# Optimization experiments

Measured on AMD Instinct MI355X. Metric: run time of the kernel, lower is better.

The kernel has to match this reference:

```python
import jax, jax.numpy as jnp
import numpy as np

N_LHB = 2097152
N_MHB = 1048576
T = 20
# Izhikevich 'RS' parameters (standard regular-spiking cell)
A, B, C, D = 0.02, 0.2, -65.0, 8.0
V_PEAK = 30.0
I_TONIC = -1.0          # set via .fill_(-1.0) in __init__
RATE_DECAY = 0.9        # EMA decay assumed for IzhikevichLayer.rate buffer
THRESH, DECAY, GAIN = 0.4, 0.998, 0.05


def setup_inputs() -> dict:
    key = jax.random.key(0)
    k1, k2 = jax.random.split(key)
    return {
        "reward": jnp.float32(0.1),
        "expected_reward": jnp.float32(0.5),
        "aversion": jnp.float32(0.3),
        "DA": jnp.float32(0.5),
        "current_goal": 1,
        "frustration": jnp.full((4,), 0.2, jnp.float32),
        "v_lhb": jnp.full((N_LHB,), C, jnp.float32),
        "u_lhb": jnp.full((N_LHB,), B * C, jnp.float32),
        "rate_lhb": jnp.zeros((N_LHB,), jnp.float32),
        "v_mhb": jnp.full((N_MHB,), C, jnp.float32),
        "u_mhb": jnp.full((N_MHB,), B * C, jnp.float32),
        "rate_mhb": jnp.zeros((N_MHB,), jnp.float32),
        "noise_lhb": jax.random.normal(k1, (T, N_LHB), jnp.float32),
        "noise_mhb": jax.random.normal(k2, (T, N_MHB), jnp.float32),
    }


def _izhikevich_run(v, u, rate, noise, i_drive):
    """Run T Izhikevich steps with per-step noise. noise: [T, n]."""
    def step(carry, n_t):
        v, u, rate = carry
        I = i_drive + I_TONIC + n_t * 0.5
        v1 = v + (0.04 * v * v + 5.0 * v + 140.0 - u + I)
        u1 = u + A * (B * v - u)
        spike = (v1 >= V_PEAK).astype(jnp.float32)
        v2 = jnp.where(spike > 0.0, C, v1)
        u2 = jnp.where(spike > 0.0, u1 + D, u1)
        rate2 = rate * RATE_DECAY + spike * (1.0 - RATE_DECAY)
        return (v2, u2, rate2), None
    (v, u, rate), _ = jax.lax.scan(step, (v, u, rate), noise)
    return rate


def reference(reward, expected_reward, aversion, DA, current_goal, frustration,
              v_lhb, u_lhb, rate_lhb, v_mhb, u_mhb, rate_mhb,
              noise_lhb, noise_mhb):
    rpe = reward - expected_reward
    disappoint = jnp.maximum(0.0, -rpe)

    rate_l = _izhikevich_run(v_lhb, u_lhb, rate_lhb, noise_lhb, disappoint * 20.0)
    rate_m = _izhikevich_run(v_mhb, u_mhb, rate_mhb, noise_mhb, aversion * 15.0)

    lhb_mean = rate_l.mean()
    mhb_mean = rate_m.mean()
    da_supp = jnp.minimum(0.5, lhb_mean * 5.0)
    ht5_supp = jnp.minimum(0.3, lhb_mean * 3.0)

    # frustration / helplessness bookkeeping (cooldown assumed 0)
    f = frustration * DECAY
    f = f.at[current_goal].add(jnp.where(rpe < -0.05, GAIN * jnp.abs(rpe), 0.0))
    f = f.at[current_goal].multiply(jnp.where(rpe > 0.1, 0.8, 1.0))
    f = jnp.clip(f, 0.0, 1.0)
    helplessness = f.max()
    switch = (f[current_goal] > THRESH).astype(jnp.float32)
    f = f.at[current_goal].multiply(jnp.where(switch > 0.0, 0.3, 1.0))

    dopa_mod = jnp.maximum(0.5, 2.0 * (1.0 - DA))
    goal_bias = f * 0.5 * dopa_mod
    explore = jnp.minimum(1.0, disappoint * 2.0 + lhb_mean * 3.0)

    scalars = jnp.stack([disappoint, da_supp, ht5_supp, lhb_mean, mhb_mean,
                         explore, helplessness, switch])
    return jnp.concatenate([scalars, goal_bias, f])  # [16]
```

## Files before the change

### kernel.cpp

```cpp
#include <hip/hip_runtime.h>

constexpr int   T       = 20;
constexpr int   N_LHB   = 2097152;
constexpr int   N_MHB   = 1048576;
constexpr float PA      = 0.02f;
constexpr float PB      = 0.2f;
constexpr float PC      = -65.0f;
constexpr float PD      = 8.0f;
constexpr float V_PEAK  = 30.0f;
constexpr float I_TONIC = -1.0f;
constexpr float RDECAY  = 0.9f;
constexpr float THRESH  = 0.4f;
constexpr float DECAY   = 0.998f;
constexpr float GAIN    = 0.05f;

constexpr int BLK   = 256;
constexpr int NB_L  = N_LHB / 4 / BLK;
constexpr int NB_M  = N_MHB / 4 / BLK;

__device__ __forceinline__ void izh_step(float& v, float& u, float& rate, float I) {
    float v1 = v + (0.04f * v * v + 5.0f * v + 140.0f - u + I);
    float u1 = u + PA * (PB * v - u);
    bool spike = (v1 >= V_PEAK);
    v = spike ? PC : v1;
    u = spike ? (u1 + PD) : u1;
    rate = rate * RDECAY + (spike ? (1.0f - RDECAY) : 0.0f);
}

__global__ __launch_bounds__(BLK) void izh_fused(
    const float* __restrict__ reward, const float* __restrict__ expected,
    const float* __restrict__ aversion,
    const float* __restrict__ v_l, const float* __restrict__ u_l, const float* __restrict__ r_l,
    const float* __restrict__ v_m, const float* __restrict__ u_m, const float* __restrict__ r_m,
    const float* __restrict__ noise_l, const float* __restrict__ noise_m,
    float* __restrict__ partial)
{
    const int bid = blockIdx.x;
    const int tid = threadIdx.x;

    const float* vv; const float* uu; const float* rr; const float* nz;
    int n4, i;
    float drive;
    if (bid < NB_L) {
        n4 = N_LHB / 4;
        i  = bid * BLK + tid;
        vv = v_l; uu = u_l; rr = r_l; nz = noise_l;
        drive = fmaxf(0.0f, expected[0] - reward[0]) * 20.0f;
    } else {
        n4 = N_MHB / 4;
        i  = (bid - NB_L) * BLK + tid;
        vv = v_m; uu = u_m; rr = r_m; nz = noise_m;
        drive = aversion[0] * 15.0f;
    }
    drive += I_TONIC;

    float4 v = ((const float4*)vv)[i];
    float4 u = ((const float4*)uu)[i];
    float4 r = ((const float4*)rr)[i];

    #pragma unroll
    for (int t = 0; t < T; ++t) {
        float4 n = ((const float4*)nz)[(size_t)t * n4 + i];
        izh_step(v.x, u.x, r.x, drive + n.x * 0.5f);
        izh_step(v.y, u.y, r.y, drive + n.y * 0.5f);
        izh_step(v.z, u.z, r.z, drive + n.z * 0.5f);
        izh_step(v.w, u.w, r.w, drive + n.w * 0.5f);
    }

    float s = (r.x + r.y) + (r.z + r.w);
    #pragma unroll
    for (int o = 32; o > 0; o >>= 1) s += __shfl_down(s, o, 64);

    __shared__ float sh[4];
    if ((tid & 63) == 0) sh[tid >> 6] = s;
    __syncthreads();
    if (tid == 0) partial[bid] = (sh[0] + sh[1]) + (sh[2] + sh[3]);
}

__global__ __launch_bounds__(BLK) void finalize(
    const float* __restrict__ partial,
    const float* __restrict__ reward, const float* __restrict__ expected,
    const float* __restrict__ aversion, const float* __restrict__ da,
    const int* __restrict__ goal, const float* __restrict__ frustration,
    float* __restrict__ out)
{
    const int tid = threadIdx.x;
    float sl = 0.0f, sm = 0.0f;
    for (int i = tid; i < NB_L; i += BLK) sl += partial[i];
    for (int i = tid; i < NB_M; i += BLK) sm += partial[NB_L + i];
    #pragma unroll
    for (int o = 32; o > 0; o >>= 1) {
        sl += __shfl_down(sl, o, 64);
        sm += __shfl_down(sm, o, 64);
    }
    __shared__ float sh[8];
    if ((tid & 63) == 0) { sh[tid >> 6] = sl; sh[4 + (tid >> 6)] = sm; }
    __syncthreads();

    if (tid == 0) {
        float lhb_sum = (sh[0] + sh[1]) + (sh[2] + sh[3]);
        float mhb_sum = (sh[4] + sh[5]) + (sh[6] + sh[7]);
        float lhb_mean = lhb_sum / (float)N_LHB;
        float mhb_mean = mhb_sum / (float)N_MHB;

        float rpe = reward[0] - expected[0];
        float disappoint = fmaxf(0.0f, -rpe);
        float da_supp = fminf(0.5f, lhb_mean * 5.0f);
        float ht5_supp = fminf(0.3f, lhb_mean * 3.0f);

        int g = goal[0];
        float f[4];
        #pragma unroll
        for (int k = 0; k < 4; ++k) f[k] = frustration[k] * DECAY;
        f[g] += (rpe < -0.05f) ? GAIN * fabsf(rpe) : 0.0f;
        f[g] *= (rpe > 0.1f) ? 0.8f : 1.0f;
        #pragma unroll
        for (int k = 0; k < 4; ++k) f[k] = fminf(1.0f, fmaxf(0.0f, f[k]));
        float helplessness = fmaxf(fmaxf(f[0], f[1]), fmaxf(f[2], f[3]));
        float sw = (f[g] > THRESH) ? 1.0f : 0.0f;
        f[g] *= (sw > 0.0f) ? 0.3f : 1.0f;

        float dopa_mod = fmaxf(0.5f, 2.0f * (1.0f - da[0]));
        float explore = fminf(1.0f, disappoint * 2.0f + lhb_mean * 3.0f);

        out[0] = disappoint;
        out[1] = da_supp;
        out[2] = ht5_supp;
        out[3] = lhb_mean;
        out[4] = mhb_mean;
        out[5] = explore;
        out[6] = helplessness;
        out[7] = sw;
        #pragma unroll
        for (int k = 0; k < 4; ++k) out[8 + k] = f[k] * 0.5f * dopa_mod;
        #pragma unroll
        for (int k = 0; k < 4; ++k) out[12 + k] = f[k];
    }
}

extern "C" void kernel_launch(void* const* d_in, const int* in_sizes, int n_in,
                              void* d_out, int out_size, void* d_ws, size_t ws_size,
                              hipStream_t stream) {
    const float* reward      = (const float*)d_in[0];
    const float* expected    = (const float*)d_in[1];
    const float* aversion    = (const float*)d_in[2];
    const float* da          = (const float*)d_in[3];
    const int*   goal        = (const int*)d_in[4];
    const float* frustration = (const float*)d_in[5];
    const float* v_l         = (const float*)d_in[6];
    const float* u_l         = (const float*)d_in[7];
    const float* r_l         = (const float*)d_in[8];
    const float* v_m         = (const float*)d_in[9];
    const float* u_m         = (const float*)d_in[10];
    const float* r_m         = (const float*)d_in[11];
    const float* noise_l     = (const float*)d_in[12];
    const float* noise_m     = (const float*)d_in[13];

    float* out     = (float*)d_out;
    float* partial = (float*)d_ws;

    izh_fused<<<NB_L + NB_M, BLK, 0, stream>>>(
        reward, expected, aversion,
        v_l, u_l, r_l, v_m, u_m, r_m,
        noise_l, noise_m, partial);

    finalize<<<1, BLK, 0, stream>>>(
        partial, reward, expected, aversion, da, goal, frustration, out);
}
```

Before: 58.46 us.

## Process eight neurons per thread, prefetch noise, and aggregate rate sums algebraically

Each thread now handles two float4 groups, which halves the block count. Noise loads are software-prefetched three timesteps ahead in registers to overlap memory latency with compute. The per-neuron rate EMA is replaced by a single per-thread EMA over the spike count, which is valid because the EMA is linear. The Izhikevich update is refactored into FMAs with folded constants. These changes cut ALU work and lengthen the memory pipeline, but they raise register pressure and may change floating-point rounding slightly.

```diff
diff --git a/kernel.cpp b/kernel.cpp
--- a/kernel.cpp
+++ b/kernel.cpp
@@ -3,28 +3,27 @@
 constexpr int   T       = 20;
 constexpr int   N_LHB   = 2097152;
 constexpr int   N_MHB   = 1048576;
-constexpr float PA      = 0.02f;
-constexpr float PB      = 0.2f;
-constexpr float PC      = -65.0f;
-constexpr float PD      = 8.0f;
 constexpr float V_PEAK  = 30.0f;
 constexpr float I_TONIC = -1.0f;
-constexpr float RDECAY  = 0.9f;
 constexpr float THRESH  = 0.4f;
 constexpr float DECAY   = 0.998f;
 constexpr float GAIN    = 0.05f;
 
-constexpr int BLK   = 256;
-constexpr int NB_L  = N_LHB / 4 / BLK;
-constexpr int NB_M  = N_MHB / 4 / BLK;
+constexpr int BLK  = 256;
+constexpr int VEC  = 8;
+constexpr int NB_L = N_LHB / (VEC * BLK);
+constexpr int NB_M = N_MHB / (VEC * BLK);
+constexpr int PF   = 3;
 
-__device__ __forceinline__ void izh_step(float& v, float& u, float& rate, float I) {
-    float v1 = v + (0.04f * v * v + 5.0f * v + 140.0f - u + I);
-    float u1 = u + PA * (PB * v - u);
-    bool spike = (v1 >= V_PEAK);
-    v = spike ? PC : v1;
-    u = spike ? (u1 + PD) : u1;
-    rate = rate * RDECAY + (spike ? (1.0f - RDECAY) : 0.0f);
+__device__ __forceinline__ float istep(float& v, float& u, float n, float c) {
+    float q  = fmaf(0.5f, n, c) - u;
+    float p  = fmaf(0.04f, v, 6.0f);
+    float v1 = fmaf(v, p, q);
+    float u1 = fmaf(0.98f, u, 0.004f * v);
+    bool  s  = (v1 >= V_PEAK);
+    v = s ? -65.0f : v1;
+    u = s ? (u1 + 8.0f) : u1;
+    return s ? 1.0f : 0.0f;
 }
 
 __global__ __launch_bounds__(BLK) void izh_fused(
@@ -38,41 +37,58 @@
     const int bid = blockIdx.x;
     const int tid = threadIdx.x;
 
-    const float* vv; const float* uu; const float* rr; const float* nz;
-    int n4, i;
+    const float4 *v4, *u4, *r4, *np;
+    int n4, ia;
     float drive;
     if (bid < NB_L) {
         n4 = N_LHB / 4;
-        i  = bid * BLK + tid;
-        vv = v_l; uu = u_l; rr = r_l; nz = noise_l;
+        ia = bid * (2 * BLK) + tid;
+        v4 = (const float4*)v_l; u4 = (const float4*)u_l; r4 = (const float4*)r_l;
+        np = (const float4*)noise_l;
         drive = fmaxf(0.0f, expected[0] - reward[0]) * 20.0f;
     } else {
         n4 = N_MHB / 4;
-        i  = (bid - NB_L) * BLK + tid;
-        vv = v_m; uu = u_m; rr = r_m; nz = noise_m;
+        ia = (bid - NB_L) * (2 * BLK) + tid;
+        v4 = (const float4*)v_m; u4 = (const float4*)u_m; r4 = (const float4*)r_m;
+        np = (const float4*)noise_m;
         drive = aversion[0] * 15.0f;
     }
-    drive += I_TONIC;
+    const int ib = ia + BLK;
+    const float c = drive + I_TONIC + 140.0f;
 
-    float4 v = ((const float4*)vv)[i];
-    float4 u = ((const float4*)uu)[i];
-    float4 r = ((const float4*)rr)[i];
+    float4 va = v4[ia], vb = v4[ib];
+    float4 ua = u4[ia], ub = u4[ib];
+    float4 ra = r4[ia], rb = r4[ib];
+
+    float S = (ra.x + ra.y) + (ra.z + ra.w) + (rb.x + rb.y) + (rb.z + rb.w);
+
+    float4 na[PF], nb[PF];
+    #pragma unroll
+    for (int t = 0; t < PF; ++t) {
+        na[t] = np[(size_t)t * n4 + ia];
+        nb[t] = np[(size_t)t * n4 + ib];
+    }
 
     #pragma unroll
     for (int t = 0; t < T; ++t) {
-        float4 n = ((const float4*)nz)[(size_t)t * n4 + i];
-        izh_step(v.x, u.x, r.x, drive + n.x * 0.5f);
-        izh_step(v.y, u.y, r.y, drive + n.y * 0.5f);
-        izh_step(v.z, u.z, r.z, drive + n.z * 0.5f);
-        izh_step(v.w, u.w, r.w, drive + n.w * 0.5f);
+        const float4 cna = na[t % PF];
+        const float4 cnb = nb[t % PF];
+        if (t + PF < T) {
+            na[t % PF] = np[(size_t)(t + PF) * n4 + ia];
+            nb[t % PF] = np[(size_t)(t + PF) * n4 + ib];
+        }
+        float cnt = istep(va.x, ua.x, cna.x, c) + istep(va.y, ua.y, cna.y, c)
+                  + istep(va.z, ua.z, cna.z, c) + istep(va.w, ua.w, cna.w, c)
+                  + istep(vb.x, ub.x, cnb.x, c) + istep(vb.y, ub.y, cnb.y, c)
+                  + istep(vb.z, ub.z, cnb.z, c) + istep(vb.w, ub.w, cnb.w, c);
+        S = fmaf(0.1f, cnt, 0.9f * S);
     }
 
-    float s = (r.x + r.y) + (r.z + r.w);
     #pragma unroll
-    for (int o = 32; o > 0; o >>= 1) s += __shfl_down(s, o, 64);
+    for (int o = 32; o > 0; o >>= 1) S += __shfl_down(S, o, 64);
 
     __shared__ float sh[4];
-    if ((tid & 63) == 0) sh[tid >> 6] = s;
+    if ((tid & 63) == 0) sh[tid >> 6] = S;
     __syncthreads();
     if (tid == 0) partial[bid] = (sh[0] + sh[1]) + (sh[2] + sh[3]);
 }
@@ -98,10 +114,8 @@
     __syncthreads();
 
     if (tid == 0) {
-        float lhb_sum = (sh[0] + sh[1]) + (sh[2] + sh[3]);
-        float mhb_sum = (sh[4] + sh[5]) + (sh[6] + sh[7]);
-        float lhb_mean = lhb_sum / (float)N_LHB;
-        float mhb_mean = mhb_sum / (float)N_MHB;
+        float lhb_mean = ((sh[0] + sh[1]) + (sh[2] + sh[3])) / (float)N_LHB;
+        float mhb_mean = ((sh[4] + sh[5]) + (sh[6] + sh[7])) / (float)N_MHB;
 
         float rpe = reward[0] - expected[0];
         float disappoint = fmaxf(0.0f, -rpe);
```

Measured after the change: 55.60 us. 1.05x faster.
